# Performance work log

Hardware: AMD Instinct MI355X
Metric: run time of the kernel (lower is better)

The kernel has to match this reference:

```python
import jax, jax.numpy as jnp
import numpy as np
import math

B, L, D = 4, 2048, 768
N_HEADS = 12
CHUNK = 8  # query_mask=1 every CHUNK tokens -> f = B*L/CHUNK, f % B == 0
VOCAB = 50000


def setup_inputs() -> dict:
    key = jax.random.key(0)
    ks = jax.random.split(key, 8)
    scale = 1.0 / math.sqrt(D)
    x_qk = jax.random.normal(ks[0], (B, L, D), jnp.float32)
    x_v = jax.random.normal(ks[1], (B, L, D), jnp.float32)
    # deterministic query mask: feature boundary every CHUNK tokens
    pos = jnp.arange(L)
    query_mask = jnp.tile((pos % CHUNK == 0).astype(jnp.int32)[None, :], (B, 1))
    input_ids = jax.random.randint(ks[2], (B, L), 2, VOCAB).astype(jnp.int64)
    # make the last 16 tokens of each row padding to exercise the pad mask
    input_ids = input_ids.at[:, -16:].set(1)
    Wq = jax.random.normal(ks[3], (D, D), jnp.float32) * scale
    Wk = jax.random.normal(ks[4], (D, D), jnp.float32) * scale
    Wv = jax.random.normal(ks[5], (D, D), jnp.float32) * scale
    Wo = jax.random.normal(ks[6], (D, D), jnp.float32) * scale
    zb = jnp.zeros((D,), jnp.float32)
    return {"x_qk": x_qk, "x_v": x_v, "query_mask": query_mask,
            "input_ids": input_ids, "pad_token_id": 1,
            "Wq": Wq, "bq": zb, "Wk": Wk, "bk": zb,
            "Wv": Wv, "bv": zb, "Wo": Wo, "bo": zb}


def reference(x_qk, x_v, query_mask, input_ids, pad_token_id,
              Wq, bq, Wk, bk, Wv, bv, Wo, bo):
    b, l, d = x_qk.shape
    n = b * l
    qm = query_mask.reshape(-1)
    f = int(np.asarray(jnp.sum(qm)))  # static feature count (f % b == 0)
    idx = jnp.nonzero(qm == 1, size=f)[0]                     # [f] query positions
    # segment boundaries: [left_i, right_i) per feature
    left = idx
    right = jnp.concatenate([idx[1:], jnp.array([n], idx.dtype)])
    pos = jnp.arange(n)
    seg_mask = (pos[None, :] >= left[:, None]) & (pos[None, :] < right[:, None])
    seg_mask = seg_mask & (input_ids.reshape(-1) != pad_token_id)[None, :]  # [f, n]

    xq = x_qk.reshape(n, d)
    xv = x_v.reshape(n, d)
    query = xq[idx]                                           # [f, d]
    q = query @ Wq.T + bq                                     # [f, d]
    k = xq @ Wk.T + bk                                        # [n, d]
    v = xv @ Wv.T + bv                                        # [n, d]

    dh = d // N_HEADS
    qh = q.reshape(f, N_HEADS, dh).transpose(1, 0, 2)         # [h, f, dh]
    kh = k.reshape(n, N_HEADS, dh).transpose(1, 0, 2)         # [h, n, dh]
    vh = v.reshape(n, N_HEADS, dh).transpose(1, 0, 2)         # [h, n, dh]

    bias = (1.0 - seg_mask.astype(jnp.float32)) * -10000.0    # [f, n]
    scores = jnp.einsum('hfd,hnd->hfn', qh, kh) / math.sqrt(dh) + bias[None]
    attn = jax.nn.softmax(scores, axis=-1)                    # [h, f, n]
    out = jnp.einsum('hfn,hnd->hfd', attn, vh)                # [h, f, dh]
    out = out.transpose(1, 0, 2).reshape(f, d)
    out = out @ Wo.T + bo
    return out.reshape(b, f // b, d)
```

## Files before the change

kernel.cpp:

```cpp
#include <hip/hip_runtime.h>

#define DMODEL 768
#define NHEADS 12
#define MAXFULL 16
#define NSTEP 24

typedef __attribute__((ext_vector_type(8))) short short8;
typedef __attribute__((ext_vector_type(4))) float f32x4;
typedef __attribute__((ext_vector_type(8))) unsigned short u16x8;

__device__ __forceinline__ unsigned pack2_bf16(float a, float b) {
  unsigned ua = __float_as_uint(a), ub = __float_as_uint(b);
  ua = (ua + 0x7fffu + ((ua >> 16) & 1u)) >> 16;
  ub = (ub + 0x7fffu + ((ub >> 16) & 1u)) & 0xffff0000u;
  return ua | ub;
}
__device__ __forceinline__ unsigned short bf16_1(float a) {
  unsigned ua = __float_as_uint(a);
  return (unsigned short)((ua + 0x7fffu + ((ua >> 16) & 1u)) >> 16);
}
__device__ __forceinline__ float b2f(unsigned short u) {
  return __uint_as_float(((unsigned)u) << 16);
}
__device__ __forceinline__ float4 lo4(u16x8 u) {
  return make_float4(b2f(u[0]), b2f(u[1]), b2f(u[2]), b2f(u[3]));
}
__device__ __forceinline__ float4 hi4(u16x8 u) {
  return make_float4(b2f(u[4]), b2f(u[5]), b2f(u[6]), b2f(u[7]));
}

__device__ __forceinline__ void load16_lds(const void* g, void* l) {
  __builtin_amdgcn_global_load_lds(
      (const __attribute__((address_space(1))) unsigned int*)g,
      (__attribute__((address_space(3))) unsigned int*)l, 16, 0, 0);
}

__global__ __launch_bounds__(256) void convAll(const float* __restrict__ w0,
    const float* __restrict__ w1, const float* __restrict__ w2,
    const float* __restrict__ w3, unsigned* __restrict__ o0,
    unsigned* __restrict__ o1, unsigned* __restrict__ o2,
    unsigned* __restrict__ o3, int wcount,
    const float* __restrict__ x0, const float* __restrict__ x1,
    unsigned* __restrict__ xo0, unsigned* __restrict__ xo1, int xcount,
    const int* __restrict__ qm, const int* __restrict__ ids,
    const int* __restrict__ padp, int n, int f, int* __restrict__ left,
    int* __restrict__ right, int* __restrict__ nvalid,
    int* __restrict__ fullrank, int* __restrict__ fullist,
    int* __restrict__ nfull) {
  __shared__ int cnt[256];
  const int t = threadIdx.x;
  if (blockIdx.x == gridDim.x - 1) {
    const int per = (n + 255) >> 8;
    const int base = t * per;
    int c = 0;
    for (int i = 0; i < per; ++i) {
      int p = base + i;
      if (p < n && qm[p] != 0) ++c;
    }
    cnt[t] = c;
    __syncthreads();
    for (int off = 1; off < 256; off <<= 1) {
      int v = (t >= off) ? cnt[t - off] : 0;
      __syncthreads();
      cnt[t] += v;
      __syncthreads();
    }
    int r = cnt[t] - c;
    for (int i = 0; i < per; ++i) {
      int p = base + i;
      if (p < n && qm[p] != 0) {
        if (r < f) left[r] = p;
        ++r;
      }
    }
    __syncthreads();
    const int pad = *padp;
    for (int i = t; i < f; i += 256) {
      int L0 = left[i];
      int R0 = (i + 1 < f) ? left[i + 1] : n;
      right[i] = R0;
      int cv = 0;
      for (int p = L0; p < R0; ++p) cv += (ids[p] != pad) ? 1 : 0;
      nvalid[i] = cv;
      fullrank[i] = -1;
    }
    __syncthreads();
    const int perf = (f + 255) >> 8;
    const int zbase = t * perf;
    int zc = 0;
    for (int i = 0; i < perf; ++i) {
      int idx = zbase + i;
      if (idx < f && nvalid[idx] == 0) ++zc;
    }
    cnt[t] = zc;
    __syncthreads();
    for (int off = 1; off < 256; off <<= 1) {
      int v = (t >= off) ? cnt[t - off] : 0;
      __syncthreads();
      cnt[t] += v;
      __syncthreads();
    }
    int zr = cnt[t] - zc;
    for (int i = 0; i < perf; ++i) {
      int idx = zbase + i;
      if (idx < f && nvalid[idx] == 0) {
        if (zr < MAXFULL) { fullist[zr] = idx; fullrank[idx] = zr; }
        ++zr;
      }
    }
    __syncthreads();
    if (t == 0) *nfull = (cnt[255] < MAXFULL) ? cnt[255] : MAXFULL;
    return;
  }
  const int nb = gridDim.x - 1;
  const int nvw = wcount >> 2;
  const float* src[4] = {w0, w1, w2, w3};
  unsigned* dst[4] = {o0, o1, o2, o3};
  for (int idx = blockIdx.x * 256 + t; idx < 4 * nvw; idx += nb * 256) {
    int m = idx / nvw, r = idx - m * nvw;
    float4 v = ((const float4*)src[m])[r];
    dst[m][2 * r]     = pack2_bf16(v.x, v.y);
    dst[m][2 * r + 1] = pack2_bf16(v.z, v.w);
  }
  const int nvx = xcount >> 2;
  for (int idx = blockIdx.x * 256 + t; idx < 2 * nvx; idx += nb * 256) {
    int m = idx / nvx, r = idx - m * nvx;
    float4 v = m ? ((const float4*)x1)[r] : ((const float4*)x0)[r];
    unsigned* d = m ? xo1 : xo0;
    d[2 * r]     = pack2_bf16(v.x, v.y);
    d[2 * r + 1] = pack2_bf16(v.z, v.w);
  }
}

struct GSeg {
  const unsigned short* A;
  const unsigned short* W;
  const float* bias;
  const int* row_map;
  void* C;
  int base;
  int nwg;
  int obf;
};

typedef unsigned short LdsTile[2][256][32];

__global__ __launch_bounds__(512, 2) void gemm256(GSeg g0, GSeg g1, GSeg g2) {
  __shared__ __attribute__((aligned(16))) LdsTile As[2];
  __shared__ __attribute__((aligned(16))) LdsTile Bs[2];
  const int t = threadIdx.x;
  const int id = blockIdx.x;
  const GSeg& d = (id >= g2.base) ? g2 : ((id >= g1.base) ? g1 : g0);
  const int lid = id - d.base;
  const int j = (d.nwg & 7) == 0 ? (lid & 7) * (d.nwg >> 3) + (lid >> 3) : lid;
  const int bn = (j % 3) * 256;
  const int bm = (j / 3) * 256;
  const int lane = t & 63, wid = t >> 6;
  const int m16 = lane & 15, quad = lane >> 4;
  const int qx = quad ^ ((m16 >> 1) & 3);
  const int wr = wid >> 2, wc = wid & 3;

  f32x4 acc[8][4];
#pragma unroll
  for (int i = 0; i < 8; ++i)
#pragma unroll
    for (int j2 = 0; j2 < 4; ++j2) acc[i][j2] = (f32x4){0.f, 0.f, 0.f, 0.f};

  const int srow = wid * 16 + (lane >> 2);
  const int skc = ((lane & 3) ^ ((lane >> 3) & 3)) * 8;
  int arow0, arow1;
  if (d.row_map) {
    arow0 = d.row_map[bm + srow];
    arow1 = d.row_map[bm + 128 + srow];
  } else {
    arow0 = bm + srow;
    arow1 = bm + 128 + srow;
  }
  const int wrow0 = bn + srow, wrow1 = bn + 128 + srow;
  const int woff0 = (wid * 16) * 32;
  const int woff1 = (128 + wid * 16) * 32;

#define STAGE256(t_, Ab, Bb) do {                                          \
    const int kk_ = (t_) * 64 + skc;                                       \
    load16_lds(d.A + (size_t)arow0 * DMODEL + kk_,      &Ab[0][0][0] + woff0); \
    load16_lds(d.A + (size_t)arow1 * DMODEL + kk_,      &Ab[0][0][0] + woff1); \
    load16_lds(d.A + (size_t)arow0 * DMODEL + kk_ + 32, &Ab[1][0][0] + woff0); \
    load16_lds(d.A + (size_t)arow1 * DMODEL + kk_ + 32, &Ab[1][0][0] + woff1); \
    load16_lds(d.W + (size_t)wrow0 * DMODEL + kk_,      &Bb[0][0][0] + woff0); \
    load16_lds(d.W + (size_t)wrow1 * DMODEL + kk_,      &Bb[0][0][0] + woff1); \
    load16_lds(d.W + (size_t)wrow0 * DMODEL + kk_ + 32, &Bb[1][0][0] + woff0); \
    load16_lds(d.W + (size_t)wrow1 * DMODEL + kk_ + 32, &Bb[1][0][0] + woff1); \
  } while (0)

#define COMPUTE256(Ab, Bb) do {                                            \
    _Pragma("unroll")                                                      \
    for (int ks = 0; ks < 2; ++ks) {                                       \
      const unsigned short* Ap = &Ab[ks][0][0];                            \
      const unsigned short* Bp = &Bb[ks][0][0];                            \
      short8 a_[8], b_[4];                                                 \
      _Pragma("unroll")                                                    \
      for (int mi = 0; mi < 8; ++mi)                                       \
        a_[mi] = *(const short8*)&Ap[(wr * 128 + mi * 16 + m16) * 32 + qx * 8]; \
      _Pragma("unroll")                                                    \
      for (int nj = 0; nj < 4; ++nj)                                       \
        b_[nj] = *(const short8*)&Bp[(wc * 64 + nj * 16 + m16) * 32 + qx * 8]; \
      __builtin_amdgcn_s_setprio(1);                                       \
      _Pragma("unroll")                                                    \
      for (int mi = 0; mi < 8; ++mi)                                       \
        _Pragma("unroll")                                                  \
        for (int nj = 0; nj < 4; ++nj)                                     \
          acc[mi][nj] = __builtin_amdgcn_mfma_f32_16x16x32_bf16(           \
              a_[mi], b_[nj], acc[mi][nj], 0, 0, 0);                       \
      __builtin_amdgcn_s_setprio(0);                                       \
    }                                                                      \
  } while (0)

  STAGE256(0, As[0], Bs[0]);
  STAGE256(1, As[1], Bs[1]);

#pragma unroll 1
  for (int g = 0; g < 5; ++g) {
    asm volatile("s_waitcnt vmcnt(8)" ::: "memory");
    __builtin_amdgcn_s_barrier();
    __builtin_amdgcn_sched_barrier(0);
    COMPUTE256(As[0], Bs[0]);
    __builtin_amdgcn_s_barrier();
    __builtin_amdgcn_sched_barrier(0);
    STAGE256(2 * g + 2, As[0], Bs[0]);
    asm volatile("s_waitcnt vmcnt(8)" ::: "memory");
    __builtin_amdgcn_s_barrier();
    __builtin_amdgcn_sched_barrier(0);
    COMPUTE256(As[1], Bs[1]);
    __builtin_amdgcn_s_barrier();
    __builtin_amdgcn_sched_barrier(0);
    STAGE256(2 * g + 3, As[1], Bs[1]);
  }
  asm volatile("s_waitcnt vmcnt(8)" ::: "memory");
  __builtin_amdgcn_s_barrier();
  __builtin_amdgcn_sched_barrier(0);
  COMPUTE256(As[0], Bs[0]);
  asm volatile("s_waitcnt vmcnt(0)" ::: "memory");
  __builtin_amdgcn_s_barrier();
  __builtin_amdgcn_sched_barrier(0);
  COMPUTE256(As[1], Bs[1]);

#undef STAGE256
#undef COMPUTE256

  float bv[4]; int bcol[4];
#pragma unroll
  for (int nj = 0; nj < 4; ++nj) {
    bcol[nj] = bn + wc * 64 + nj * 16 + m16;
    bv[nj] = d.bias[bcol[nj]];
  }
  if (d.obf) {
    unsigned short* Cb = (unsigned short*)d.C;
#pragma unroll
    for (int mi = 0; mi < 8; ++mi) {
      const int rbase = bm + wr * 128 + mi * 16 + quad * 4;
#pragma unroll
      for (int r = 0; r < 4; ++r) {
        const int row = rbase + r;
#pragma unroll
        for (int nj = 0; nj < 4; ++nj)
          Cb[(size_t)row * DMODEL + bcol[nj]] = bf16_1(acc[mi][nj][r] + bv[nj]);
      }
    }
  } else {
    float* Cf = (float*)d.C;
#pragma unroll
    for (int mi = 0; mi < 8; ++mi) {
      const int rbase = bm + wr * 128 + mi * 16 + quad * 4;
#pragma unroll
      for (int r = 0; r < 4; ++r) {
        const int row = rbase + r;
#pragma unroll
        for (int nj = 0; nj < 4; ++nj)
          Cf[(size_t)row * DMODEL + bcol[nj]] = acc[mi][nj][r] + bv[nj];
      }
    }
  }
}

__global__ __launch_bounds__(64) void gemmWo(const unsigned short* __restrict__ A,
    const unsigned short* __restrict__ W, const float* __restrict__ bias,
    float* __restrict__ C) {
  __shared__ __attribute__((aligned(16))) unsigned short As[4][64 * 32];
  __shared__ __attribute__((aligned(16))) unsigned short Bs[4][64 * 32];
  const int bid = blockIdx.x;
  const int bm = (bid / 12) * 64, bn = (bid % 12) * 64;
  const int lane = threadIdx.x;
  const int m16 = lane & 15, quad = lane >> 4;
  const int qx = quad ^ ((m16 >> 1) & 3);
  const int srow = lane >> 2;
  const int skc = ((lane & 3) ^ ((lane >> 3) & 3)) * 8;

  f32x4 acc[4][4];
#pragma unroll
  for (int i = 0; i < 4; ++i)
#pragma unroll
    for (int j2 = 0; j2 < 4; ++j2) acc[i][j2] = (f32x4){0.f, 0.f, 0.f, 0.f};

#define STAGEW(s_, t_) do {                                                \
    const int kk_ = (t_) * 32 + skc;                                       \
    _Pragma("unroll")                                                      \
    for (int i_ = 0; i_ < 4; ++i_) {                                       \
      load16_lds(A + (size_t)(bm + 16 * i_ + srow) * DMODEL + kk_,         \
                 &As[s_][i_ * 16 * 32]);                                   \
      load16_lds(W + (size_t)(bn + 16 * i_ + srow) * DMODEL + kk_,         \
                 &Bs[s_][i_ * 16 * 32]);                                   \
    }                                                                      \
  } while (0)

#define COMPUTEW(s_) do {                                                  \
    short8 a_[4], b_[4];                                                   \
    _Pragma("unroll")                                                      \
    for (int mi = 0; mi < 4; ++mi)                                         \
      a_[mi] = *(const short8*)&As[s_][(mi * 16 + m16) * 32 + qx * 8];     \
    _Pragma("unroll")                                                      \
    for (int nj = 0; nj < 4; ++nj)                                         \
      b_[nj] = *(const short8*)&Bs[s_][(nj * 16 + m16) * 32 + qx * 8];     \
    _Pragma("unroll")                                                      \
    for (int mi = 0; mi < 4; ++mi)                                         \
      _Pragma("unroll")                                                    \
      for (int nj = 0; nj < 4; ++nj)                                       \
        acc[mi][nj] = __builtin_amdgcn_mfma_f32_16x16x32_bf16(             \
            a_[mi], b_[nj], acc[mi][nj], 0, 0, 0);                         \
  } while (0)

  STAGEW(0, 0); STAGEW(1, 1); STAGEW(2, 2); STAGEW(3, 3);

#pragma unroll 1
  for (int ts = 0; ts < NSTEP - 4; ++ts) {
    asm volatile("s_waitcnt vmcnt(24)" ::: "memory");
    __builtin_amdgcn_sched_barrier(0);
    COMPUTEW(ts & 3);
    asm volatile("s_waitcnt lgkmcnt(0)" ::: "memory");
    __builtin_amdgcn_sched_barrier(0);
    STAGEW(ts & 3, ts + 4);
  }
  asm volatile("s_waitcnt vmcnt(24)" ::: "memory");
  __builtin_amdgcn_sched_barrier(0);
  COMPUTEW(0);
  asm volatile("s_waitcnt vmcnt(16)" ::: "memory");
  __builtin_amdgcn_sched_barrier(0);
  COMPUTEW(1);
  asm volatile("s_waitcnt vmcnt(8)" ::: "memory");
  __builtin_amdgcn_sched_barrier(0);
  COMPUTEW(2);
  asm volatile("s_waitcnt vmcnt(0)" ::: "memory");
  __builtin_amdgcn_sched_barrier(0);
  COMPUTEW(3);

#undef STAGEW
#undef COMPUTEW

  float bv[4]; int bcol[4];
#pragma unroll
  for (int nj = 0; nj < 4; ++nj) {
    bcol[nj] = bn + nj * 16 + m16;
    bv[nj] = bias[bcol[nj]];
  }
#pragma unroll
  for (int mi = 0; mi < 4; ++mi) {
    const int rbase = bm + mi * 16 + quad * 4;
#pragma unroll
    for (int r = 0; r < 4; ++r) {
      const int row = rbase + r;
#pragma unroll
      for (int nj = 0; nj < 4; ++nj)
        C[(size_t)row * DMODEL + bcol[nj]] = acc[mi][nj][r] + bv[nj];
    }
  }
}

__device__ __forceinline__ float allreduce64(float x) {
#pragma unroll
  for (int m = 1; m < 64; m <<= 1) x += __shfl_xor(x, m, 64);
  return x;
}

__global__ __launch_bounds__(256) void attn_all(const float* __restrict__ q,
    const unsigned short* __restrict__ k, const unsigned short* __restrict__ v,
    const int* __restrict__ left, const int* __restrict__ right,
    const int* __restrict__ nvalid, const int* __restrict__ ids,
    const int* __restrict__ padp, unsigned short* __restrict__ out,
    const int* __restrict__ fullist, const int* __restrict__ nfullp,
    int n, int f, int P, int nfx, float* __restrict__ pm,
    float* __restrict__ pl, float* __restrict__ pacc) {
  __shared__ float q_lds[4][8 * 64];
  __shared__ float w_lds[4][64 * 8];
  const int x = blockIdx.x, lane = threadIdx.x & 63, wid = threadIdx.x >> 6;
  const int h = blockIdx.y * 4 + wid;

  if (x < nfx) {
    const int f0 = x * 4;
    const int off = h * 64 + lane;
    const int pad = *padp;
    int L0[4], R0[4], nv[4];
#pragma unroll
    for (int ff = 0; ff < 4; ++ff) {
      L0[ff] = left[f0 + ff];
      R0[ff] = right[f0 + ff];
      nv[ff] = nvalid[f0 + ff];
    }
    bool allfast = true;
#pragma unroll
    for (int ff = 0; ff < 4; ++ff) allfast &= (R0[ff] - L0[ff] == 8);
    if (allfast) {
      float qv[4], kv[4][8], vv[4][8];
      unsigned live[4];
#pragma unroll
      for (int ff = 0; ff < 4; ++ff) {
        qv[ff] = q[(size_t)(f0 + ff) * DMODEL + off];
        live[ff] = 0;
#pragma unroll
        for (int p = 0; p < 8; ++p) {
          kv[ff][p] = b2f(k[(size_t)(L0[ff] + p) * DMODEL + off]);
          vv[ff][p] = b2f(v[(size_t)(L0[ff] + p) * DMODEL + off]);
          live[ff] |= (ids[L0[ff] + p] != pad ? 1u : 0u) << p;
        }
      }
      float s[4][8];
#pragma unroll
      for (int ff = 0; ff < 4; ++ff)
#pragma unroll
        for (int p = 0; p < 8; ++p) s[ff][p] = qv[ff] * kv[ff][p];
#pragma unroll
      for (int m_ = 1; m_ < 64; m_ <<= 1)
#pragma unroll
        for (int ff = 0; ff < 4; ++ff)
#pragma unroll
          for (int p = 0; p < 8; ++p) s[ff][p] += __shfl_xor(s[ff][p], m_, 64);
#pragma unroll
      for (int ff = 0; ff < 4; ++ff) {
        if (nv[ff] == 0) continue;
        float mx = -1e30f;
#pragma unroll
        for (int p = 0; p < 8; ++p) {
          s[ff][p] = ((live[ff] >> p) & 1u) ? s[ff][p] * 0.125f : -1e30f;
          mx = fmaxf(mx, s[ff][p]);
        }
        float l = 0.f, acc = 0.f;
#pragma unroll
        for (int p = 0; p < 8; ++p) {
          float w = __expf(s[ff][p] - mx);
          l += w;
          acc += w * vv[ff][p];
        }
        out[(size_t)(f0 + ff) * DMODEL + off] = bf16_1(acc / l);
      }
      return;
    }
    for (int ff = 0; ff < 4; ++ff) {
      if (nv[ff] == 0) continue;
      const float qv = q[(size_t)(f0 + ff) * DMODEL + off];
      float m = -1e30f, l = 0.f, acc = 0.f;
      for (int p = L0[ff]; p < R0[ff]; ++p) {
        if (ids[p] == pad) continue;
        float s = allreduce64(qv * b2f(k[(size_t)p * DMODEL + off])) * 0.125f;
        float mn = fmaxf(m, s);
        float al = __expf(m - mn);
        float w = __expf(s - mn);
        l = l * al + w;
        acc = acc * al + w * b2f(v[(size_t)p * DMODEL + off]);
        m = mn;
      }
      out[(size_t)(f0 + ff) * DMODEL + off] = bf16_1(acc / l);
    }
    return;
  }

  const int nfull = *nfullp;
  if (nfull == 0) return;
  const int piece = x - nfx;
  const int pk = n / P;

#pragma unroll
  for (int fl = 0; fl < 8; ++fl)
    q_lds[wid][fl * 64 + lane] =
        (fl < nfull) ? q[(size_t)fullist[fl] * DMODEL + h * 64 + lane] : 0.f;

  float m[8], l[8], acc[8];
#pragma unroll
  for (int f_ = 0; f_ < 8; ++f_) { m[f_] = -1e30f; l[f_] = 0.f; acc[f_] = 0.f; }

  for (int c = 0; c < pk; c += 64) {
    const int pc = piece * pk + c;
    float s[8];
#pragma unroll
    for (int f_ = 0; f_ < 8; ++f_) s[f_] = 0.f;
    const u16x8* kp = (const u16x8*)(k + (size_t)(pc + lane) * DMODEL + h * 64);
#pragma unroll 1
    for (int g = 0; g < 2; ++g) {
      u16x8 u0 = kp[g * 4 + 0], u1 = kp[g * 4 + 1], u2 = kp[g * 4 + 2],
            u3 = kp[g * 4 + 3];
      float4 kv0 = lo4(u0), kv1 = hi4(u0), kv2 = lo4(u1), kv3 = hi4(u1),
             kv4 = lo4(u2), kv5 = hi4(u2), kv6 = lo4(u3), kv7 = hi4(u3);
      const float4* qb = (const float4*)&q_lds[wid][g * 32];
#pragma unroll
      for (int f_ = 0; f_ < 8; ++f_) {
        float4 q0 = qb[f_ * 16 + 0], q1 = qb[f_ * 16 + 1], q2 = qb[f_ * 16 + 2],
               q3 = qb[f_ * 16 + 3], q4 = qb[f_ * 16 + 4], q5 = qb[f_ * 16 + 5],
               q6 = qb[f_ * 16 + 6], q7 = qb[f_ * 16 + 7];
        float acc0 = q0.x * kv0.x + q0.y * kv0.y + q0.z * kv0.z + q0.w * kv0.w;
        acc0 += q1.x * kv1.x + q1.y * kv1.y + q1.z * kv1.z + q1.w * kv1.w;
        acc0 += q2.x * kv2.x + q2.y * kv2.y + q2.z * kv2.z + q2.w * kv2.w;
        acc0 += q3.x * kv3.x + q3.y * kv3.y + q3.z * kv3.z + q3.w * kv3.w;
        acc0 += q4.x * kv4.x + q4.y * kv4.y + q4.z * kv4.z + q4.w * kv4.w;
        acc0 += q5.x * kv5.x + q5.y * kv5.y + q5.z * kv5.z + q5.w * kv5.w;
        acc0 += q6.x * kv6.x + q6.y * kv6.y + q6.z * kv6.z + q6.w * kv6.w;
        acc0 += q7.x * kv7.x + q7.y * kv7.y + q7.z * kv7.z + q7.w * kv7.w;
        s[f_] += acc0;
      }
    }
    float mx[8];
#pragma unroll
    for (int f_ = 0; f_ < 8; ++f_) mx[f_] = s[f_] * 0.125f;
#pragma unroll
    for (int f_ = 0; f_ < 8; ++f_) s[f_] = mx[f_];
#pragma unroll
    for (int st = 1; st < 64; st <<= 1)
#pragma unroll
      for (int f_ = 0; f_ < 8; ++f_) mx[f_] = fmaxf(mx[f_], __shfl_xor(mx[f_], st, 64));
    float alpha[8], w[8], sum[8];
#pragma unroll
    for (int f_ = 0; f_ < 8; ++f_) {
      float mn = fmaxf(m[f_], mx[f_]);
      alpha[f_] = __expf(m[f_] - mn);
      w[f_] = __expf(s[f_] - mn);
      m[f_] = mn;
      sum[f_] = w[f_];
    }
#pragma unroll
    for (int st = 1; st < 64; st <<= 1)
#pragma unroll
      for (int f_ = 0; f_ < 8; ++f_) sum[f_] += __shfl_xor(sum[f_], st, 64);
#pragma unroll
    for (int f_ = 0; f_ < 8; ++f_) l[f_] = l[f_] * alpha[f_] + sum[f_];
    *(float4*)&w_lds[wid][lane * 8]     = make_float4(w[0], w[1], w[2], w[3]);
    *(float4*)&w_lds[wid][lane * 8 + 4] = make_float4(w[4], w[5], w[6], w[7]);
#pragma unroll
    for (int f_ = 0; f_ < 8; ++f_) acc[f_] *= alpha[f_];
    const unsigned short* vb = v + (size_t)pc * DMODEL + h * 64 + lane;
#pragma unroll 4
    for (int kk = 0; kk < 64; ++kk) {
      float vd = b2f(vb[(size_t)kk * DMODEL]);
      float4 wa = *(const float4*)&w_lds[wid][kk * 8];
      float4 wb = *(const float4*)&w_lds[wid][kk * 8 + 4];
      acc[0] += wa.x * vd; acc[1] += wa.y * vd; acc[2] += wa.z * vd; acc[3] += wa.w * vd;
      acc[4] += wb.x * vd; acc[5] += wb.y * vd; acc[6] += wb.z * vd; acc[7] += wb.w * vd;
    }
  }

  for (int f_ = 0; f_ < nfull; ++f_) {
    size_t idx = ((size_t)f_ * NHEADS + h) * P + piece;
    if (lane == 0) { pm[idx] = m[f_]; pl[idx] = l[f_]; }
    pacc[idx * 64 + lane] = acc[f_];
  }
}

__global__ __launch_bounds__(256) void attn_full_comb(
    const int* __restrict__ fullist, const int* __restrict__ nfullp,
    int P, const float* __restrict__ pm, const float* __restrict__ pl,
    const float* __restrict__ pacc, unsigned short* __restrict__ out) {
  const int fl = blockIdx.x, h = blockIdx.y;
  if (fl >= *nfullp) return;
  const int feat = fullist[fl];
  const int t = threadIdx.x, lane = t & 63, wv = t >> 6;
  const size_t base = ((size_t)fl * NHEADS + h) * P;

  __shared__ float s_pm[128];
  __shared__ float s_sc[128];
  __shared__ float s_red[4];
  __shared__ float s_part[4][64];

  for (int sp = t; sp < P; sp += 256) s_pm[sp] = pm[base + sp];
  __syncthreads();
  float mloc = -1e30f;
  for (int sp = t; sp < P; sp += 256) mloc = fmaxf(mloc, s_pm[sp]);
#pragma unroll
  for (int st = 1; st < 64; st <<= 1) mloc = fmaxf(mloc, __shfl_xor(mloc, st, 64));
  if (lane == 0) s_red[wv] = mloc;
  __syncthreads();
  const float M = fmaxf(fmaxf(s_red[0], s_red[1]), fmaxf(s_red[2], s_red[3]));
  __syncthreads();
  float lloc = 0.f;
  for (int sp = t; sp < P; sp += 256) {
    float sc = __expf(s_pm[sp] - M);
    s_sc[sp] = sc;
    lloc += pl[base + sp] * sc;
  }
#pragma unroll
  for (int st = 1; st < 64; st <<= 1) lloc += __shfl_xor(lloc, st, 64);
  if (lane == 0) s_red[wv] = lloc;
  __syncthreads();
  const float Lt = s_red[0] + s_red[1] + s_red[2] + s_red[3];
  float At = 0.f;
  for (int sp = wv; sp < P; sp += 4)
    At += pacc[(base + sp) * 64 + lane] * s_sc[sp];
  s_part[wv][lane] = At;
  __syncthreads();
  if (wv == 0) {
    float tot = s_part[0][lane] + s_part[1][lane] + s_part[2][lane] + s_part[3][lane];
    out[(size_t)feat * DMODEL + h * 64 + lane] = bf16_1(tot / Lt);
  }
}

extern "C" void kernel_launch(void* const* d_in, const int* in_sizes, int n_in,
                              void* d_out, int out_size, void* d_ws, size_t ws_size,
                              hipStream_t stream) {
  const float* x_qk = (const float*)d_in[0];
  const float* x_v  = (const float*)d_in[1];
  const int* qm     = (const int*)d_in[2];
  const int* ids    = (const int*)d_in[3];
  const int* padp   = (const int*)d_in[4];
  const float* Wq = (const float*)d_in[5];
  const float* bq = (const float*)d_in[6];
  const float* Wk = (const float*)d_in[7];
  const float* bk = (const float*)d_in[8];
  const float* Wv = (const float*)d_in[9];
  const float* bv = (const float*)d_in[10];
  const float* Wo = (const float*)d_in[11];
  const float* bo = (const float*)d_in[12];

  const int n = in_sizes[0] / DMODEL;
  const int f = out_size / DMODEL;

  unsigned short* kfh = (unsigned short*)d_ws;
  unsigned short* vfh = kfh + (size_t)n * DMODEL;
  float* qf = (float*)(vfh + (size_t)n * DMODEL);
  unsigned short* af = (unsigned short*)(qf + (size_t)f * DMODEL);
  unsigned short* wqb = af + (size_t)f * DMODEL;
  unsigned short* wkb = wqb + DMODEL * DMODEL;
  unsigned short* wvb = wkb + DMODEL * DMODEL;
  unsigned short* wob = wvb + DMODEL * DMODEL;
  unsigned short* xqb = wob + DMODEL * DMODEL;
  unsigned short* xvb = xqb + (size_t)n * DMODEL;
  int* left     = (int*)(xvb + (size_t)n * DMODEL);
  int* right    = left + f;
  int* nvalid   = right + f;
  int* fullrank = nvalid + f;
  int* fullist  = fullrank + f;
  int* nfull    = fullist + MAXFULL;
  size_t off_bytes = ((size_t)((char*)(nfull + 1) - (char*)d_ws) + 255) & ~(size_t)255;
  int P = 128;
  while (P > 16) {
    size_t need = (size_t)MAXFULL * NHEADS * P * 66 * sizeof(float);
    if (off_bytes + need <= ws_size && (n / P) % 64 == 0 && n % P == 0) break;
    P >>= 1;
  }
  float* pm = (float*)((char*)d_ws + off_bytes);
  float* pl = pm + (size_t)MAXFULL * NHEADS * P;
  float* pacc = pl + (size_t)MAXFULL * NHEADS * P;

  convAll<<<2049, 256, 0, stream>>>(Wq, Wk, Wv, Wo, (unsigned*)wqb,
                                    (unsigned*)wkb, (unsigned*)wvb,
                                    (unsigned*)wob, DMODEL * DMODEL,
                                    x_qk, x_v, (unsigned*)xqb, (unsigned*)xvb,
                                    n * DMODEL,
                                    qm, ids, padp, n, f, left, right, nvalid,
                                    fullrank, fullist, nfull);

  const int TKV256 = 3 * (n / 256);
  const int TF256  = 3 * (f / 256);
  GSeg g0 = { xqb, wkb, bk, nullptr, (void*)kfh, 0,           TKV256, 1 };
  GSeg g1 = { xvb, wvb, bv, nullptr, (void*)vfh, TKV256,      TKV256, 1 };
  GSeg g2 = { xqb, wqb, bq, left,    (void*)qf,  2 * TKV256,  TF256,  0 };
  gemm256<<<2 * TKV256 + TF256, 512, 0, stream>>>(g0, g1, g2);

  const int nfx = f / 4;
  attn_all<<<dim3(nfx + P, NHEADS / 4), 256, 0, stream>>>(qf, kfh, vfh, left,
                                                          right, nvalid, ids,
                                                          padp, af, fullist,
                                                          nfull, n, f, P, nfx,
                                                          pm, pl, pacc);
  attn_full_comb<<<dim3(MAXFULL, NHEADS), 256, 0, stream>>>(fullist, nfull, P,
                                                            pm, pl, pacc, af);

  gemmWo<<<(f / 64) * (DMODEL / 64), 64, 0, stream>>>(af, wob, bo, (float*)d_out);
}
```

Measured before the change: 214.2 us.

## Fuse activation fp32-to-bf16 conversion into the projection GEMM A-operand load

Removes the separate pass that converted x_qk and x_v to bf16 in the prep kernel and the workspace buffers it used. The GEMM now reads fp32 activations straight into registers one tile ahead, packs them to bf16 and writes them to LDS before each compute step. Only the weight B operand keeps the direct global-to-LDS load. This avoids a full write and re-read of the bf16 activation copies, but doubles the A-operand bytes fetched by the GEMM and adds register pressure and LDS write work inside the main loop.

```diff
diff --git a/kernel.cpp b/kernel.cpp
--- a/kernel.cpp
+++ b/kernel.cpp
@@ -40,8 +40,6 @@
     const float* __restrict__ w3, unsigned* __restrict__ o0,
     unsigned* __restrict__ o1, unsigned* __restrict__ o2,
     unsigned* __restrict__ o3, int wcount,
-    const float* __restrict__ x0, const float* __restrict__ x1,
-    unsigned* __restrict__ xo0, unsigned* __restrict__ xo1, int xcount,
     const int* __restrict__ qm, const int* __restrict__ ids,
     const int* __restrict__ padp, int n, int f, int* __restrict__ left,
     int* __restrict__ right, int* __restrict__ nvalid,
@@ -122,18 +120,10 @@
     dst[m][2 * r]     = pack2_bf16(v.x, v.y);
     dst[m][2 * r + 1] = pack2_bf16(v.z, v.w);
   }
-  const int nvx = xcount >> 2;
-  for (int idx = blockIdx.x * 256 + t; idx < 2 * nvx; idx += nb * 256) {
-    int m = idx / nvx, r = idx - m * nvx;
-    float4 v = m ? ((const float4*)x1)[r] : ((const float4*)x0)[r];
-    unsigned* d = m ? xo1 : xo0;
-    d[2 * r]     = pack2_bf16(v.x, v.y);
-    d[2 * r + 1] = pack2_bf16(v.z, v.w);
-  }
 }
 
 struct GSeg {
-  const unsigned short* A;
+  const float* A;
   const unsigned short* W;
   const float* bias;
   const int* row_map;
@@ -179,17 +169,42 @@
   const int wrow0 = bn + srow, wrow1 = bn + 128 + srow;
   const int woff0 = (wid * 16) * 32;
   const int woff1 = (128 + wid * 16) * 32;
-
-#define STAGE256(t_, Ab, Bb) do {                                          \
+  const int wd0 = (woff0 >> 1) + lane * 4;
+  const int wd1 = (woff1 >> 1) + lane * 4;
+
+  float4 rA[8], rB[8];
+
+#define STAGEB(t_, Bb) do {                                                \
     const int kk_ = (t_) * 64 + skc;                                       \
-    load16_lds(d.A + (size_t)arow0 * DMODEL + kk_,      &Ab[0][0][0] + woff0); \
-    load16_lds(d.A + (size_t)arow1 * DMODEL + kk_,      &Ab[0][0][0] + woff1); \
-    load16_lds(d.A + (size_t)arow0 * DMODEL + kk_ + 32, &Ab[1][0][0] + woff0); \
-    load16_lds(d.A + (size_t)arow1 * DMODEL + kk_ + 32, &Ab[1][0][0] + woff1); \
     load16_lds(d.W + (size_t)wrow0 * DMODEL + kk_,      &Bb[0][0][0] + woff0); \
     load16_lds(d.W + (size_t)wrow1 * DMODEL + kk_,      &Bb[0][0][0] + woff1); \
     load16_lds(d.W + (size_t)wrow0 * DMODEL + kk_ + 32, &Bb[1][0][0] + woff0); \
     load16_lds(d.W + (size_t)wrow1 * DMODEL + kk_ + 32, &Bb[1][0][0] + woff1); \
+  } while (0)
+
+#define ISSUEA(P, t_) do {                                                 \
+    const size_t r0_ = (size_t)arow0 * DMODEL + (t_) * 64 + skc;           \
+    const size_t r1_ = (size_t)arow1 * DMODEL + (t_) * 64 + skc;           \
+    P[0] = *(const float4*)&d.A[r0_];      P[1] = *(const float4*)&d.A[r0_ + 4];  \
+    P[2] = *(const float4*)&d.A[r1_];      P[3] = *(const float4*)&d.A[r1_ + 4];  \
+    P[4] = *(const float4*)&d.A[r0_ + 32]; P[5] = *(const float4*)&d.A[r0_ + 36]; \
+    P[6] = *(const float4*)&d.A[r1_ + 32]; P[7] = *(const float4*)&d.A[r1_ + 36]; \
+  } while (0)
+
+#define WRITEA(P, Ab) do {                                                 \
+    unsigned* wp_;                                                         \
+    wp_ = (unsigned*)(&Ab[0][0][0]) + wd0;                                 \
+    wp_[0] = pack2_bf16(P[0].x, P[0].y); wp_[1] = pack2_bf16(P[0].z, P[0].w); \
+    wp_[2] = pack2_bf16(P[1].x, P[1].y); wp_[3] = pack2_bf16(P[1].z, P[1].w); \
+    wp_ = (unsigned*)(&Ab[0][0][0]) + wd1;                                 \
+    wp_[0] = pack2_bf16(P[2].x, P[2].y); wp_[1] = pack2_bf16(P[2].z, P[2].w); \
+    wp_[2] = pack2_bf16(P[3].x, P[3].y); wp_[3] = pack2_bf16(P[3].z, P[3].w); \
+    wp_ = (unsigned*)(&Ab[1][0][0]) + wd0;                                 \
+    wp_[0] = pack2_bf16(P[4].x, P[4].y); wp_[1] = pack2_bf16(P[4].z, P[4].w); \
+    wp_[2] = pack2_bf16(P[5].x, P[5].y); wp_[3] = pack2_bf16(P[5].z, P[5].w); \
+    wp_ = (unsigned*)(&Ab[1][0][0]) + wd1;                                 \
+    wp_[0] = pack2_bf16(P[6].x, P[6].y); wp_[1] = pack2_bf16(P[6].z, P[6].w); \
+    wp_[2] = pack2_bf16(P[7].x, P[7].y); wp_[3] = pack2_bf16(P[7].z, P[7].w); \
   } while (0)
 
 #define COMPUTE256(Ab, Bb) do {                                            \
@@ -215,37 +230,34 @@
     }                                                                      \
   } while (0)
 
-  STAGE256(0, As[0], Bs[0]);
-  STAGE256(1, As[1], Bs[1]);
+#define TILE(P, Ab, Bb, VM)                                                \
+    asm volatile("s_waitcnt vmcnt(" #VM ")" ::: "memory");                 \
+    WRITEA(P, Ab);                                                         \
+    asm volatile("s_waitcnt lgkmcnt(0)" ::: "memory");                     \
+    __builtin_amdgcn_s_barrier();                                          \
+    __builtin_amdgcn_sched_barrier(0);                                     \
+    COMPUTE256(Ab, Bb);                                                    \
+    __builtin_amdgcn_s_barrier();                                          \
+    __builtin_amdgcn_sched_barrier(0);
+
+  STAGEB(0, Bs[0]); ISSUEA(rA, 0);
+  STAGEB(1, Bs[1]); ISSUEA(rB, 1);
 
 #pragma unroll 1
   for (int g = 0; g < 5; ++g) {
-    asm volatile("s_waitcnt vmcnt(8)" ::: "memory");
-    __builtin_amdgcn_s_barrier();
-    __builtin_amdgcn_sched_barrier(0);
-    COMPUTE256(As[0], Bs[0]);
-    __builtin_amdgcn_s_barrier();
-    __builtin_amdgcn_sched_barrier(0);
-    STAGE256(2 * g + 2, As[0], Bs[0]);
-    asm volatile("s_waitcnt vmcnt(8)" ::: "memory");
-    __builtin_amdgcn_s_barrier();
-    __builtin_amdgcn_sched_barrier(0);
-    COMPUTE256(As[1], Bs[1]);
-    __builtin_amdgcn_s_barrier();
-    __builtin_amdgcn_sched_barrier(0);
-    STAGE256(2 * g + 3, As[1], Bs[1]);
-  }
-  asm volatile("s_waitcnt vmcnt(8)" ::: "memory");
-  __builtin_amdgcn_s_barrier();
-  __builtin_amdgcn_sched_barrier(0);
-  COMPUTE256(As[0], Bs[0]);
-  asm volatile("s_waitcnt vmcnt(0)" ::: "memory");
-  __builtin_amdgcn_s_barrier();
-  __builtin_amdgcn_sched_barrier(0);
-  COMPUTE256(As[1], Bs[1]);
-
-#undef STAGE256
+    TILE(rA, As[0], Bs[0], 12)
+    STAGEB(2 * g + 2, Bs[0]); ISSUEA(rA, 2 * g + 2);
+    TILE(rB, As[1], Bs[1], 12)
+    STAGEB(2 * g + 3, Bs[1]); ISSUEA(rB, 2 * g + 3);
+  }
+  TILE(rA, As[0], Bs[0], 12)
+  TILE(rB, As[1], Bs[1], 0)
+
+#undef STAGEB
+#undef ISSUEA
+#undef WRITEA
 #undef COMPUTE256
+#undef TILE
 
   float bv[4]; int bcol[4];
 #pragma unroll
@@ -635,9 +647,7 @@
   unsigned short* wkb = wqb + DMODEL * DMODEL;
   unsigned short* wvb = wkb + DMODEL * DMODEL;
   unsigned short* wob = wvb + DMODEL * DMODEL;
-  unsigned short* xqb = wob + DMODEL * DMODEL;
-  unsigned short* xvb = xqb + (size_t)n * DMODEL;
-  int* left     = (int*)(xvb + (size_t)n * DMODEL);
+  int* left     = (int*)(wob + DMODEL * DMODEL);
   int* right    = left + f;
   int* nvalid   = right + f;
   int* fullrank = nvalid + f;
@@ -654,19 +664,17 @@
   float* pl = pm + (size_t)MAXFULL * NHEADS * P;
   float* pacc = pl + (size_t)MAXFULL * NHEADS * P;
 
-  convAll<<<2049, 256, 0, stream>>>(Wq, Wk, Wv, Wo, (unsigned*)wqb,
-                                    (unsigned*)wkb, (unsigned*)wvb,
-                                    (unsigned*)wob, DMODEL * DMODEL,
-                                    x_qk, x_v, (unsigned*)xqb, (unsigned*)xvb,
-                                    n * DMODEL,
-                                    qm, ids, padp, n, f, left, right, nvalid,
-                                    fullrank, fullist, nfull);
+  convAll<<<257, 256, 0, stream>>>(Wq, Wk, Wv, Wo, (unsigned*)wqb,
+                                   (unsigned*)wkb, (unsigned*)wvb,
+                                   (unsigned*)wob, DMODEL * DMODEL,
+                                   qm, ids, padp, n, f, left, right, nvalid,
+                                   fullrank, fullist, nfull);
 
   const int TKV256 = 3 * (n / 256);
   const int TF256  = 3 * (f / 256);
-  GSeg g0 = { xqb, wkb, bk, nullptr, (void*)kfh, 0,           TKV256, 1 };
-  GSeg g1 = { xvb, wvb, bv, nullptr, (void*)vfh, TKV256,      TKV256, 1 };
-  GSeg g2 = { xqb, wqb, bq, left,    (void*)qf,  2 * TKV256,  TF256,  0 };
+  GSeg g0 = { x_qk, wkb, bk, nullptr, (void*)kfh, 0,           TKV256, 1 };
+  GSeg g1 = { x_v,  wvb, bv, nullptr, (void*)vfh, TKV256,      TKV256, 1 };
+  GSeg g2 = { x_qk, wqb, bq, left,    (void*)qf,  2 * TKV256,  TF256,  0 };
   gemm256<<<2 * TKV256 + TF256, 512, 0, stream>>>(g0, g1, g2);
 
   const int nfx = f / 4;
```

New measurement: 409.7 us. 1.91x slower.
